# Optimization experiments

Measured on AMD Instinct MI355X. Metric: run time of the kernel, lower is better.

The kernel has to match this reference:

```python
import jax, jax.numpy as jnp
import numpy as np

N_NODES = 100000
EMB_DIM = 64
HIDDEN = 8
OUT_DIM = 16
NUM_HEADS = 3
B = 1024
E_RAND = 3200000


def setup_inputs() -> dict:
    key = jax.random.key(0)
    ks = jax.random.split(key, 12)
    src = jax.random.randint(ks[0], (E_RAND,), 0, N_NODES, dtype=jnp.int32)
    dst = jax.random.randint(ks[1], (E_RAND,), 0, N_NODES, dtype=jnp.int32)
    loop = jnp.arange(N_NODES, dtype=jnp.int32)
    src = jnp.concatenate([src, loop])
    dst = jnp.concatenate([dst, loop])
    # multi-hot query indicator, ~50 items per query, guarantee >=1 item
    queries = (jax.random.uniform(ks[2], (B, N_NODES)) < 5e-4).astype(jnp.float32)
    queries = queries.at[:, 0].set(1.0)
    pos_items = jax.random.randint(ks[3], (B,), 0, N_NODES, dtype=jnp.int32)
    neg_items = jax.random.randint(ks[4], (B,), 0, N_NODES, dtype=jnp.int32)
    embedding = jax.random.normal(ks[5], (N_NODES, EMB_DIM), dtype=jnp.float32) * 0.1
    # GAT layer 1: NUM_HEADS heads, in=64 -> out=8 per head (concat)
    W1 = jax.random.normal(ks[6], (NUM_HEADS, EMB_DIM, HIDDEN), dtype=jnp.float32) * 0.1
    a1 = jax.random.normal(ks[7], (NUM_HEADS, 2 * HIDDEN), dtype=jnp.float32) * 0.1
    # GAT layer 2: 1 head, in=24 -> out=16
    W2 = jax.random.normal(ks[8], (NUM_HEADS * HIDDEN, OUT_DIM), dtype=jnp.float32) * 0.1
    a2 = jax.random.normal(ks[9], (2 * OUT_DIM,), dtype=jnp.float32) * 0.1
    return {"queries": queries, "pos_items": pos_items, "neg_items": neg_items,
            "embedding": embedding, "W1": W1, "a1": a1, "W2": W2, "a2": a2,
            "src": src, "dst": dst}


def gat_layer(h, W, a, src, dst, n_nodes):
    # h: [N, in], W: [H, in, o], a: [H, 2o]; returns [N, H, o]
    o = W.shape[-1]
    z = jnp.einsum('nd,hdo->nho', h, W)            # [N,H,o]
    zs, zd = z[src], z[dst]                         # [E,H,o]
    e = jax.nn.leaky_relu(
        jnp.einsum('eho,ho->eh', zs, a[:, :o]) +
        jnp.einsum('eho,ho->eh', zd, a[:, o:]), 0.01)  # [E,H]
    m = jax.ops.segment_max(e, dst, num_segments=n_nodes)       # [N,H]
    alpha = jnp.exp(e - m[dst])                                  # [E,H]
    denom = jax.ops.segment_sum(alpha, dst, num_segments=n_nodes)
    num = jax.ops.segment_sum(alpha[:, :, None] * zs, dst, num_segments=n_nodes)
    return num / denom[:, :, None]


def gat_forward(embedding, W1, a1, W2, a2, src, dst):
    n = embedding.shape[0]
    h1 = gat_layer(embedding, W1, a1, src, dst, n)       # [N,H,hid]
    h1 = jax.nn.elu(h1.reshape(n, -1))                   # [N,H*hid]
    h2 = gat_layer(h1, W2[None], a2[None], src, dst, n)  # [N,1,out]
    return h2[:, 0]                                      # [N,out]


def reference(queries, pos_items, neg_items, embedding, W1, a1, W2, a2, src, dst):
    item_embeds = gat_forward(embedding, W1, a1, W2, a2, src, dst)  # [N,16]
    item_cnt = jnp.sum(queries, axis=1)                              # [B]
    query_embeds = jnp.matmul(queries, item_embeds) / item_cnt[:, None]
    pos_embed = item_embeds[pos_items]
    neg_embed = item_embeds[neg_items]
    return (query_embeds, pos_embed, neg_embed)
```

## Files before the change

### kernel.cpp

```cpp
#include <hip/hip_runtime.h>
#include <hip/hip_fp16.h>

#define NH 3
#define HID 8
#define C1 24
#define C2 16
#define BSH 5
#define BNODES 32
#define NBMAX 3200
#define SCAP 1792
#define PCHUNK 16384
#define AZS 32
#define QCAP 512

__device__ inline float2 cvt2(unsigned u) {
    __half2 h;
    *reinterpret_cast<unsigned*>(&h) = u;
    return __half22float2(h);
}

__global__ __launch_bounds__(256) void k_z1(
    const float* __restrict__ emb, const float* __restrict__ W1g,
    const float* __restrict__ a1g, __half* __restrict__ az1h,
    float4* __restrict__ f1d, int* __restrict__ bcnt, int NB, int N) {
    __shared__ float sW[NH * 64 * HID];
    __shared__ float sa[NH * 2 * HID];
    for (int i = threadIdx.x; i < NH * 64 * HID; i += blockDim.x) sW[i] = W1g[i];
    for (int i = threadIdx.x; i < NH * 2 * HID; i += blockDim.x) sa[i] = a1g[i];
    int n = blockIdx.x * blockDim.x + threadIdx.x;
    if (n < NB) bcnt[n] = 0;
    __syncthreads();
    if (n >= N) return;
    float e[64];
    const float4* ep = (const float4*)(emb + (size_t)n * 64);
#pragma unroll
    for (int i = 0; i < 16; ++i) {
        float4 v = ep[i];
        e[4*i+0] = v.x; e[4*i+1] = v.y; e[4*i+2] = v.z; e[4*i+3] = v.w;
    }
    float z[C1];
#pragma unroll
    for (int c = 0; c < C1; ++c) z[c] = 0.f;
    for (int d = 0; d < 64; ++d) {
        float ed = e[d];
#pragma unroll
        for (int h = 0; h < NH; ++h) {
            const float4* wp = (const float4*)&sW[(h * 64 + d) * HID];
            float4 w0 = wp[0], w1 = wp[1];
            z[h*HID+0] += ed * w0.x; z[h*HID+1] += ed * w0.y;
            z[h*HID+2] += ed * w0.z; z[h*HID+3] += ed * w0.w;
            z[h*HID+4] += ed * w1.x; z[h*HID+5] += ed * w1.y;
            z[h*HID+6] += ed * w1.z; z[h*HID+7] += ed * w1.w;
        }
    }
    float fs[NH], fd[NH];
#pragma unroll
    for (int h = 0; h < NH; ++h) {
        float s = 0.f, dsum = 0.f;
#pragma unroll
        for (int o = 0; o < HID; ++o) {
            s    += z[h*HID+o] * sa[h*2*HID + o];
            dsum += z[h*HID+o] * sa[h*2*HID + HID + o];
        }
        fs[h] = s; fd[h] = dsum;
    }
    __half hb[32];
    hb[0] = __float2half_rn(fs[0]); hb[1] = __float2half_rn(fs[1]);
    hb[2] = __float2half_rn(fs[2]); hb[3] = __half(0.f);
#pragma unroll
    for (int o = 0; o < C1; ++o) hb[4 + o] = __float2half_rn(z[o]);
#pragma unroll
    for (int o = 28; o < 32; ++o) hb[o] = __half(0.f);
    uint4* zo = (uint4*)(az1h + ((size_t)n << 5));
    const uint4* hbu = (const uint4*)hb;
    zo[0] = hbu[0]; zo[1] = hbu[1]; zo[2] = hbu[2]; zo[3] = hbu[3];
    f1d[n] = make_float4(fd[0], fd[1], fd[2], 0.f);
}

__global__ __launch_bounds__(256) void k_count(const int* __restrict__ dst,
                                               int* __restrict__ bcnt, int E, int NB) {
    __shared__ int lh[NBMAX];
    for (int i = threadIdx.x; i < NB; i += 256) lh[i] = 0;
    __syncthreads();
    int base = blockIdx.x * PCHUNK;
    int end = base + PCHUNK; if (end > E) end = E;
    for (int i = base + threadIdx.x; i < end; i += 256)
        atomicAdd(&lh[dst[i] >> BSH], 1);
    __syncthreads();
    for (int i = threadIdx.x; i < NB; i += 256)
        if (lh[i]) atomicAdd(&bcnt[i], lh[i]);
}

#define SCANK 13
__global__ __launch_bounds__(256) void k_bscan(const int* __restrict__ bcnt,
                                               int* __restrict__ boff,
                                               int* __restrict__ bcur,
                                               int* __restrict__ rowptr,
                                               int NB, int N, int E) {
    __shared__ int sd[256];
    int tid = threadIdx.x;
    int v[SCANK]; int tsum = 0;
#pragma unroll
    for (int i = 0; i < SCANK; ++i) {
        int g = tid * SCANK + i;
        v[i] = (g < NB) ? bcnt[g] : 0;
        tsum += v[i];
    }
    sd[tid] = tsum; __syncthreads();
    for (int off = 1; off < 256; off <<= 1) {
        int t = (tid >= off) ? sd[tid - off] : 0;
        __syncthreads();
        sd[tid] += t;
        __syncthreads();
    }
    int pref = sd[tid] - tsum;
#pragma unroll
    for (int i = 0; i < SCANK; ++i) {
        int g = tid * SCANK + i;
        if (g < NB) { boff[g] = pref; bcur[g] = pref; pref += v[i]; }
    }
    if (tid == 255) boff[NB] = pref;
    if (tid == 0) rowptr[N] = E;
}

__global__ __launch_bounds__(256) void k_part(const int* __restrict__ src,
                                              const int* __restrict__ dst,
                                              int* __restrict__ bcur,
                                              int* __restrict__ bedges, int E, int NB) {
    __shared__ int lh[NBMAX];
    __shared__ int lbase[NBMAX];
    for (int i = threadIdx.x; i < NB; i += 256) lh[i] = 0;
    __syncthreads();
    int base = blockIdx.x * PCHUNK;
    int end = base + PCHUNK; if (end > E) end = E;
    for (int i = base + threadIdx.x; i < end; i += 256)
        atomicAdd(&lh[dst[i] >> BSH], 1);
    __syncthreads();
    for (int i = threadIdx.x; i < NB; i += 256) {
        int c = lh[i];
        lbase[i] = c ? atomicAdd(&bcur[i], c) : 0;
        lh[i] = 0;
    }
    __syncthreads();
    for (int i = base + threadIdx.x; i < end; i += 256) {
        int d = dst[i];
        int b = d >> BSH;
        int p = lbase[b] + atomicAdd(&lh[b], 1);
        bedges[p] = src[i] | ((d & (BNODES - 1)) << 17);
    }
}

__global__ __launch_bounds__(256) void k_gat1(
    const int* __restrict__ boff, int* __restrict__ bedges,
    const __half* __restrict__ az1h, const float4* __restrict__ f1d,
    const float* __restrict__ W2g, const float* __restrict__ a2g,
    __half* __restrict__ z2h, float* __restrict__ f2s, float* __restrict__ f2d,
    int* __restrict__ rowptr,
    const float* __restrict__ queries, int* __restrict__ qnz,
    float* __restrict__ qval, int* __restrict__ qcnt,
    int NB, int N) {
    __shared__ int ssrc[SCAP];
    __shared__ int scnt[BNODES];
    __shared__ int sstart[BNODES + 1];
    __shared__ int scur[BNODES];
    __shared__ float sW2[C1 * C2];
    __shared__ float sa2[2 * C2];
    __shared__ float sagg[BNODES * 28];
    int tid = threadIdx.x;
    int b = blockIdx.x;

    if (b >= NB) {
        int qb = b - NB;
        __shared__ int qn;
        if (tid == 0) qn = 0;
        __syncthreads();
        const float4* qrow = (const float4*)(queries + (size_t)qb * N);
        int n4 = N >> 2;
        for (int i = tid; i < n4; i += 256) {
            float4 v = qrow[i];
            float vv[4] = {v.x, v.y, v.z, v.w};
#pragma unroll
            for (int c = 0; c < 4; ++c) {
                if (vv[c] != 0.f) {
                    int p = atomicAdd(&qn, 1);
                    if (p < QCAP) {
                        qnz[(size_t)qb * QCAP + p] = i * 4 + c;
                        qval[(size_t)qb * QCAP + p] = vv[c];
                    }
                }
            }
        }
        __syncthreads();
        if (tid == 0) qcnt[qb] = qn < QCAP ? qn : QCAP;
        return;
    }

    int beg = boff[b], cnt = boff[b + 1] - beg;
    if (tid < BNODES) scnt[tid] = 0;
    for (int i = tid; i < C1 * C2; i += 256) sW2[i] = W2g[i];
    if (tid < 2 * C2) sa2[tid] = a2g[tid];
    __syncthreads();
    for (int i = tid; i < cnt; i += 256)
        atomicAdd(&scnt[bedges[beg + i] >> 17], 1);
    __syncthreads();
    if (tid < BNODES) {
        int v = scnt[tid];
        int x = v;
        for (int d = 1; d < BNODES; d <<= 1) {
            int t = __shfl_up(x, d, 64);
            if (tid >= d) x += t;
        }
        sstart[tid] = x - v;
        scur[tid] = x - v;
        if (tid == BNODES - 1) sstart[BNODES] = x;
    }
    __syncthreads();
    for (int i = tid; i < cnt; i += 256) {
        int pk = bedges[beg + i];
        int p = atomicAdd(&scur[pk >> 17], 1);
        ssrc[p] = pk & 0x1FFFF;
    }
    __syncthreads();
    for (int i = tid; i < cnt; i += 256) bedges[beg + i] = ssrc[i];
    int n0 = b << BSH;
    if (tid < BNODES) rowptr[n0 + tid] = beg + sstart[tid];

    int nl = tid >> 3;
    int g  = (tid >> 2) & 1;
    int q  = tid & 3;
    int lane = tid & 63;
    int base4 = lane & ~3;
    int n = n0 + nl;
    int s0 = sstart[nl], s1 = sstart[nl + 1];
    float4 fdv = f1d[n];
    float accLo[4], accHi[4];
#pragma unroll
    for (int j = 0; j < 4; ++j) { accLo[j] = 0.f; accHi[j] = 0.f; }
    float den0 = 0.f, den1 = 0.f, den2 = 0.f;
    bool q1f = (q == 1), q2f = (q == 2), q3f = (q == 3), q0f = (q == 0);
    for (int i = s0 + g; i < s1; i += 2) {
        int s = ssrc[i];
        uint4 u = *((const uint4*)(az1h + ((size_t)s << 5)) + q);
        float2 v0 = cvt2(u.x), v1 = cvt2(u.y), v2 = cvt2(u.z), v3 = cvt2(u.w);
        float e0 = v0.x + fdv.x, e1 = v0.y + fdv.y, e2 = v1.x + fdv.z;
        e0 = e0 > 0.f ? e0 : 0.01f * e0;
        e1 = e1 > 0.f ? e1 : 0.01f * e1;
        e2 = e2 > 0.f ? e2 : 0.01f * e2;
        float a0 = __expf(e0), a1 = __expf(e1), a2 = __expf(e2);
        float b0 = __shfl(a0, base4, 64);
        float b1 = __shfl(a1, base4, 64);
        float b2 = __shfl(a2, base4, 64);
        den0 += b0; den1 += b1; den2 += b2;
        float cLo = q1f ? b0 : (q2f ? b1 : (q3f ? b2 : 0.f));
        float cHi = q0f ? b0 : (q1f ? b1 : (q2f ? b2 : 0.f));
        accLo[0] += cLo * v0.x; accLo[1] += cLo * v0.y;
        accLo[2] += cLo * v1.x; accLo[3] += cLo * v1.y;
        accHi[0] += cHi * v2.x; accHi[1] += cHi * v2.y;
        accHi[2] += cHi * v3.x; accHi[3] += cHi * v3.y;
    }
#pragma unroll
    for (int j = 0; j < 4; ++j) {
        accLo[j] += __shfl_xor(accLo[j], 4, 64);
        accHi[j] += __shfl_xor(accHi[j], 4, 64);
    }
    den0 += __shfl_xor(den0, 4, 64);
    den1 += __shfl_xor(den1, 4, 64);
    den2 += __shfl_xor(den2, 4, 64);
    if (g == 0) {
        float* sg = &sagg[nl * 28];
        if (q > 0) {
#pragma unroll
            for (int j = 0; j < 4; ++j) sg[q * 8 - 4 + j] = accLo[j];
        }
        if (q < 3) {
#pragma unroll
            for (int j = 0; j < 4; ++j) sg[q * 8 + j] = accHi[j];
        }
        if (q == 0) { sg[24] = den0; sg[25] = den1; sg[26] = den2; }
    }
    __syncthreads();
    if (tid < BNODES) {
        const float* sg = &sagg[tid * 28];
        int nn = n0 + tid;
        float h1v[C1];
        float inv0 = 1.f / sg[24], inv1 = 1.f / sg[25], inv2 = 1.f / sg[26];
#pragma unroll
        for (int o = 0; o < HID; ++o) {
            float v0 = sg[o] * inv0;
            float v1 = sg[HID + o] * inv1;
            float v2 = sg[2 * HID + o] * inv2;
            h1v[o]           = v0 > 0.f ? v0 : (__expf(v0) - 1.f);
            h1v[HID + o]     = v1 > 0.f ? v1 : (__expf(v1) - 1.f);
            h1v[2 * HID + o] = v2 > 0.f ? v2 : (__expf(v2) - 1.f);
        }
        float zz[C2];
#pragma unroll
        for (int k = 0; k < C2; ++k) zz[k] = 0.f;
        for (int c = 0; c < C1; ++c) {
            float hv = h1v[c];
#pragma unroll
            for (int k = 0; k < C2; ++k) zz[k] += hv * sW2[c * C2 + k];
        }
        float fs = 0.f, fdd = 0.f;
#pragma unroll
        for (int k = 0; k < C2; ++k) {
            fs  += zz[k] * sa2[k];
            fdd += zz[k] * sa2[C2 + k];
        }
        __half zb[16];
#pragma unroll
        for (int k = 0; k < C2; ++k) zb[k] = __float2half_rn(zz[k]);
        uint4* zo = (uint4*)(z2h + ((size_t)nn << 4));
        const uint4* zbu = (const uint4*)zb;
        zo[0] = zbu[0]; zo[1] = zbu[1];
        f2s[nn] = fs;
        f2d[nn] = fdd;
    }
}

__global__ __launch_bounds__(256) void k_gat2(
    const int* __restrict__ rowptr, const int* __restrict__ csr,
    const __half* __restrict__ z2h, const float* __restrict__ f2s,
    const float* __restrict__ f2d, float* __restrict__ item, int N) {
    int t = blockIdx.x * blockDim.x + threadIdx.x;
    int n = t >> 3;
    if (n >= N) return;
    int q  = t & 1;
    int g  = (t >> 1) & 3;
    int beg = rowptr[n], end = rowptr[n + 1];
    float fdv = f2d[n];
    float acc[8];
#pragma unroll
    for (int j = 0; j < 8; ++j) acc[j] = 0.f;
    float den = 0.f;
    for (int i = beg + g; i < end; i += 4) {
        int s = csr[i];
        float e = f2s[s] + fdv;
        e = e > 0.f ? e : 0.01f * e;
        float a = __expf(e);
        den += a;
        uint4 u = *((const uint4*)(z2h + ((size_t)s << 4)) + q);
        float2 v0 = cvt2(u.x), v1 = cvt2(u.y), v2 = cvt2(u.z), v3 = cvt2(u.w);
        acc[0] += a * v0.x; acc[1] += a * v0.y;
        acc[2] += a * v1.x; acc[3] += a * v1.y;
        acc[4] += a * v2.x; acc[5] += a * v2.y;
        acc[6] += a * v3.x; acc[7] += a * v3.y;
    }
#pragma unroll
    for (int j = 0; j < 8; ++j) {
        acc[j] += __shfl_xor(acc[j], 2, 64);
        acc[j] += __shfl_xor(acc[j], 4, 64);
    }
    den += __shfl_xor(den, 2, 64);
    den += __shfl_xor(den, 4, 64);
    if ((t & 6) == 0) {
        float inv = 1.f / den;
        float4* io = (float4*)(item + (size_t)n * C2 + q * 8);
        io[0] = make_float4(acc[0]*inv, acc[1]*inv, acc[2]*inv, acc[3]*inv);
        io[1] = make_float4(acc[4]*inv, acc[5]*inv, acc[6]*inv, acc[7]*inv);
    }
}

__global__ __launch_bounds__(256) void k_final(
    const float* __restrict__ item, const int* __restrict__ qnz,
    const float* __restrict__ qval, const int* __restrict__ qcnt,
    const int* __restrict__ pos, const int* __restrict__ neg,
    float* __restrict__ out, int B) {
    int b = blockIdx.x;
    int cnt = qcnt[b];
    float acc[C2];
#pragma unroll
    for (int k = 0; k < C2; ++k) acc[k] = 0.f;
    float wsum = 0.f;
    for (int i = threadIdx.x; i < cnt; i += 256) {
        int idx = qnz[(size_t)b * QCAP + i];
        float qv = qval[(size_t)b * QCAP + i];
        wsum += qv;
        const float4* rp = (const float4*)(item + (size_t)idx * C2);
        float4 r0 = rp[0], r1 = rp[1], r2 = rp[2], r3 = rp[3];
        acc[0]  += qv*r0.x; acc[1]  += qv*r0.y; acc[2]  += qv*r0.z; acc[3]  += qv*r0.w;
        acc[4]  += qv*r1.x; acc[5]  += qv*r1.y; acc[6]  += qv*r1.z; acc[7]  += qv*r1.w;
        acc[8]  += qv*r2.x; acc[9]  += qv*r2.y; acc[10] += qv*r2.z; acc[11] += qv*r2.w;
        acc[12] += qv*r3.x; acc[13] += qv*r3.y; acc[14] += qv*r3.z; acc[15] += qv*r3.w;
    }
    __shared__ float red[4][C2 + 1];
    int lane = threadIdx.x & 63, wid = threadIdx.x >> 6;
#pragma unroll
    for (int k = 0; k < C2; ++k)
        for (int off = 32; off; off >>= 1) acc[k] += __shfl_down(acc[k], off, 64);
    for (int off = 32; off; off >>= 1) wsum += __shfl_down(wsum, off, 64);
    if (lane == 0) {
#pragma unroll
        for (int k = 0; k < C2; ++k) red[wid][k] = acc[k];
        red[wid][C2] = wsum;
    }
    __syncthreads();
    if (threadIdx.x < C2 + 1) {
        float s = red[0][threadIdx.x] + red[1][threadIdx.x] +
                  red[2][threadIdx.x] + red[3][threadIdx.x];
        red[0][threadIdx.x] = s;
    }
    __syncthreads();
    if (threadIdx.x < C2)
        out[(size_t)b * C2 + threadIdx.x] = red[0][threadIdx.x] / red[0][C2];
    else if (threadIdx.x >= 64 && threadIdx.x < 64 + C2)
        out[((size_t)B + b) * C2 + (threadIdx.x - 64)] =
            item[(size_t)pos[b] * C2 + (threadIdx.x - 64)];
    else if (threadIdx.x >= 128 && threadIdx.x < 128 + C2)
        out[((size_t)2 * B + b) * C2 + (threadIdx.x - 128)] =
            item[(size_t)neg[b] * C2 + (threadIdx.x - 128)];
}

extern "C" void kernel_launch(void* const* d_in, const int* in_sizes, int n_in,
                              void* d_out, int out_size, void* d_ws, size_t ws_size,
                              hipStream_t stream) {
    const float* queries = (const float*)d_in[0];
    const int*   pos     = (const int*)d_in[1];
    const int*   neg     = (const int*)d_in[2];
    const float* emb     = (const float*)d_in[3];
    const float* W1      = (const float*)d_in[4];
    const float* a1      = (const float*)d_in[5];
    const float* W2      = (const float*)d_in[6];
    const float* a2      = (const float*)d_in[7];
    const int*   src     = (const int*)d_in[8];
    const int*   dst     = (const int*)d_in[9];

    int B = in_sizes[1];
    int N = in_sizes[3] / 64;
    int E = in_sizes[8];
    float* out = (float*)d_out;

    int NB = (N + BNODES - 1) >> BSH;

    char* w = (char*)d_ws;
    auto alloc = [&](size_t bytes) -> char* {
        char* p = w;
        w += (bytes + 255) & ~(size_t)255;
        return p;
    };
    __half* az1h   = (__half*)alloc(sizeof(__half) * (size_t)N * AZS);
    float4* f1d    = (float4*)alloc(sizeof(float4) * (size_t)N);
    __half* z2h    = (__half*)alloc(sizeof(__half) * (size_t)N * C2);
    float*  f2s    = (float*)alloc(sizeof(float) * (size_t)N);
    float*  f2d    = (float*)alloc(sizeof(float) * (size_t)N);
    float*  item   = (float*)alloc(sizeof(float) * (size_t)N * C2);
    int*    bcnt   = (int*)alloc(sizeof(int) * (size_t)NB);
    int*    boff   = (int*)alloc(sizeof(int) * (size_t)(NB + 1));
    int*    bcur   = (int*)alloc(sizeof(int) * (size_t)NB);
    int*    rowptr = (int*)alloc(sizeof(int) * (size_t)(N + 1));
    int*    bedges = (int*)alloc(sizeof(int) * (size_t)E);
    int*    qnz    = (int*)alloc(sizeof(int) * (size_t)B * QCAP);
    float*  qval   = (float*)alloc(sizeof(float) * (size_t)B * QCAP);
    int*    qcnt   = (int*)alloc(sizeof(int) * (size_t)B);

    int nblkN = (N + 255) / 256;
    int nPart = (E + PCHUNK - 1) / PCHUNK;

    k_z1<<<nblkN, 256, 0, stream>>>(emb, W1, a1, az1h, f1d, bcnt, NB, N);
    k_count<<<nPart, 256, 0, stream>>>(dst, bcnt, E, NB);
    k_bscan<<<1, 256, 0, stream>>>(bcnt, boff, bcur, rowptr, NB, N, E);
    k_part<<<nPart, 256, 0, stream>>>(src, dst, bcur, bedges, E, NB);
    k_gat1<<<NB + B, 256, 0, stream>>>(boff, bedges, az1h, f1d, W2, a2,
                                       z2h, f2s, f2d, rowptr,
                                       queries, qnz, qval, qcnt, NB, N);
    k_gat2<<<(N * 8 + 255) / 256, 256, 0, stream>>>(rowptr, bedges, z2h, f2s, f2d, item, N);
    k_final<<<B, 256, 0, stream>>>(item, qnz, qval, qcnt, pos, neg, out, B);
}
```

Baseline: 813.9 us.

## Split query scan across both GAT kernels and stage per-block edges in LDS

The dense query-row scan (about 400 MB of reads) is split in half. One half runs as leading blocks of k_gat1 and the other as leading blocks of k_gat2, so the bandwidth-bound scan overlaps with the gather-heavy GAT work in both kernels. k_gat2 is rewritten to use one block per 32-node bucket. Each block loads the bucket's source list and row offsets into shared memory before the per-node softmax aggregation, instead of reading the global CSR directly. The new k_gat2 has no bounds guard for a partial last bucket, so it relies on N being a multiple of 32. It also adds shared-memory use that may limit occupancy.

New measurement: 803.2 us, median of 2. About the same (-1.3%).

```diff
diff --git a/kernel.cpp b/kernel.cpp
--- a/kernel.cpp
+++ b/kernel.cpp
@@ -19,6 +19,33 @@
     return __half22float2(h);
 }
 
+__device__ inline void qscan_row(const float* __restrict__ queries,
+                                 int* __restrict__ qnz, float* __restrict__ qval,
+                                 int* __restrict__ qcnt, int qb, int N) {
+    __shared__ int qn;
+    int tid = threadIdx.x;
+    if (tid == 0) qn = 0;
+    __syncthreads();
+    const float4* qrow = (const float4*)(queries + (size_t)qb * N);
+    int n4 = N >> 2;
+    for (int i = tid; i < n4; i += 256) {
+        float4 v = qrow[i];
+        float vv[4] = {v.x, v.y, v.z, v.w};
+#pragma unroll
+        for (int c = 0; c < 4; ++c) {
+            if (vv[c] != 0.f) {
+                int p = atomicAdd(&qn, 1);
+                if (p < QCAP) {
+                    qnz[(size_t)qb * QCAP + p] = i * 4 + c;
+                    qval[(size_t)qb * QCAP + p] = vv[c];
+                }
+            }
+        }
+    }
+    __syncthreads();
+    if (tid == 0) qcnt[qb] = qn < QCAP ? qn : QCAP;
+}
+
 __global__ __launch_bounds__(256) void k_z1(
     const float* __restrict__ emb, const float* __restrict__ W1g,
     const float* __restrict__ a1g, __half* __restrict__ az1h,
@@ -158,7 +185,12 @@
     int* __restrict__ rowptr,
     const float* __restrict__ queries, int* __restrict__ qnz,
     float* __restrict__ qval, int* __restrict__ qcnt,
-    int NB, int N) {
+    int QB, int N) {
+    int tid = threadIdx.x;
+    int b = blockIdx.x;
+    if (b < QB) { qscan_row(queries, qnz, qval, qcnt, b, N); return; }
+    b -= QB;
+
     __shared__ int ssrc[SCAP];
     __shared__ int scnt[BNODES];
     __shared__ int sstart[BNODES + 1];
@@ -166,34 +198,6 @@
     __shared__ float sW2[C1 * C2];
     __shared__ float sa2[2 * C2];
     __shared__ float sagg[BNODES * 28];
-    int tid = threadIdx.x;
-    int b = blockIdx.x;
-
-    if (b >= NB) {
-        int qb = b - NB;
-        __shared__ int qn;
-        if (tid == 0) qn = 0;
-        __syncthreads();
-        const float4* qrow = (const float4*)(queries + (size_t)qb * N);
-        int n4 = N >> 2;
-        for (int i = tid; i < n4; i += 256) {
-            float4 v = qrow[i];
-            float vv[4] = {v.x, v.y, v.z, v.w};
-#pragma unroll
-            for (int c = 0; c < 4; ++c) {
-                if (vv[c] != 0.f) {
-                    int p = atomicAdd(&qn, 1);
-                    if (p < QCAP) {
-                        qnz[(size_t)qb * QCAP + p] = i * 4 + c;
-                        qval[(size_t)qb * QCAP + p] = vv[c];
-                    }
-                }
-            }
-        }
-        __syncthreads();
-        if (tid == 0) qcnt[qb] = qn < QCAP ? qn : QCAP;
-        return;
-    }
 
     int beg = boff[b], cnt = boff[b + 1] - beg;
     if (tid < BNODES) scnt[tid] = 0;
@@ -319,22 +323,38 @@
 }
 
 __global__ __launch_bounds__(256) void k_gat2(
-    const int* __restrict__ rowptr, const int* __restrict__ csr,
+    const int* __restrict__ boff, const int* __restrict__ bedges,
+    const int* __restrict__ rowptr,
     const __half* __restrict__ z2h, const float* __restrict__ f2s,
-    const float* __restrict__ f2d, float* __restrict__ item, int N) {
-    int t = blockIdx.x * blockDim.x + threadIdx.x;
-    int n = t >> 3;
-    if (n >= N) return;
-    int q  = t & 1;
-    int g  = (t >> 1) & 3;
-    int beg = rowptr[n], end = rowptr[n + 1];
+    const float* __restrict__ f2d, float* __restrict__ item,
+    const float* __restrict__ queries, int* __restrict__ qnz,
+    float* __restrict__ qval, int* __restrict__ qcnt,
+    int QB0, int QB, int N) {
+    int tid = threadIdx.x;
+    int b = blockIdx.x;
+    if (b < QB) { qscan_row(queries, qnz, qval, qcnt, QB0 + b, N); return; }
+    b -= QB;
+
+    __shared__ int ssrc[SCAP];
+    __shared__ int sstart[BNODES + 1];
+    int n0 = b << BSH;
+    int beg = boff[b], cnt = boff[b + 1] - beg;
+    if (tid <= BNODES) sstart[tid] = rowptr[n0 + tid] - beg;
+    for (int i = tid; i < cnt; i += 256) ssrc[i] = bedges[beg + i];
+    __syncthreads();
+
+    int nl = tid >> 3;
+    int q  = tid & 1;
+    int g  = (tid >> 1) & 3;
+    int n = n0 + nl;
+    int s0 = sstart[nl], s1 = sstart[nl + 1];
     float fdv = f2d[n];
     float acc[8];
 #pragma unroll
     for (int j = 0; j < 8; ++j) acc[j] = 0.f;
     float den = 0.f;
-    for (int i = beg + g; i < end; i += 4) {
-        int s = csr[i];
+    for (int i = s0 + g; i < s1; i += 4) {
+        int s = ssrc[i];
         float e = f2s[s] + fdv;
         e = e > 0.f ? e : 0.01f * e;
         float a = __expf(e);
@@ -353,7 +373,7 @@
     }
     den += __shfl_xor(den, 2, 64);
     den += __shfl_xor(den, 4, 64);
-    if ((t & 6) == 0) {
+    if (g == 0) {
         float inv = 1.f / den;
         float4* io = (float4*)(item + (size_t)n * C2 + q * 8);
         io[0] = make_float4(acc[0]*inv, acc[1]*inv, acc[2]*inv, acc[3]*inv);
@@ -431,6 +451,7 @@
     float* out = (float*)d_out;
 
     int NB = (N + BNODES - 1) >> BSH;
+    int QB1 = B / 2, QB2 = B - QB1;
 
     char* w = (char*)d_ws;
     auto alloc = [&](size_t bytes) -> char* {
@@ -460,9 +481,10 @@
     k_count<<<nPart, 256, 0, stream>>>(dst, bcnt, E, NB);
     k_bscan<<<1, 256, 0, stream>>>(bcnt, boff, bcur, rowptr, NB, N, E);
     k_part<<<nPart, 256, 0, stream>>>(src, dst, bcur, bedges, E, NB);
-    k_gat1<<<NB + B, 256, 0, stream>>>(boff, bedges, az1h, f1d, W2, a2,
-                                       z2h, f2s, f2d, rowptr,
-                                       queries, qnz, qval, qcnt, NB, N);
-    k_gat2<<<(N * 8 + 255) / 256, 256, 0, stream>>>(rowptr, bedges, z2h, f2s, f2d, item, N);
+    k_gat1<<<QB1 + NB, 256, 0, stream>>>(boff, bedges, az1h, f1d, W2, a2,
+                                         z2h, f2s, f2d, rowptr,
+                                         queries, qnz, qval, qcnt, QB1, N);
+    k_gat2<<<QB2 + NB, 256, 0, stream>>>(boff, bedges, rowptr, z2h, f2s, f2d, item,
+                                         queries, qnz, qval, qcnt, QB1, QB2, N);
     k_final<<<B, 256, 0, stream>>>(item, qnz, qval, qcnt, pos, neg, out, B);
 }
```
